# Kernel optimization log

Measured on AMD Instinct MI355X. Metric: run time of the kernel, lower is better.

Reference implementation:

```python
import jax, jax.numpy as jnp
import numpy as np

N_NODES = 100000
VOCAB = 5000
D = 256            # embedding_size
L = 4              # num_gnn_layers
E2 = 300000        # arity-2 hyperedges
E3 = 200000        # arity-3 hyperedges
T = 2000           # target nodes
N_LIN = 2          # num_linear_layer
EPS = 1e-5


def setup_inputs() -> dict:
    key = jax.random.key(0)
    ks = jax.random.split(key, 18)
    s = 0.02
    inp = {
        'x': jax.random.randint(ks[0], (N_NODES,), 0, VOCAB, dtype=jnp.int64) if jax.config.jax_enable_x64 else jax.random.randint(ks[0], (N_NODES,), 0, VOCAB).astype(jnp.int32),
        'edge_index': jax.random.randint(ks[1], (2, 500000), 0, N_NODES).astype(jnp.int32),
        'edge_list_arity2': jax.random.randint(ks[2], (2, E2), 0, N_NODES).astype(jnp.int32),
        'edge_list_arity3': jax.random.randint(ks[3], (3, E3), 0, N_NODES).astype(jnp.int32),
        'target_indices': jax.random.randint(ks[4], (T,), 0, N_NODES).astype(jnp.int32),
        # learned parameters
        'emb': jax.random.normal(ks[5], (VOCAB, D), jnp.float32),
        'W_root': jax.random.normal(ks[6], (L, D, D), jnp.float32) * s,
        'W_e2': jax.random.normal(ks[7], (L, 2 * D, 2 * D), jnp.float32) * s,
        'W_e3': jax.random.normal(ks[8], (L, 3 * D, 3 * D), jnp.float32) * s,
        'ln_g': jnp.ones((L, D), jnp.float32),
        'ln_b': jnp.zeros((L, D), jnp.float32),
        'reg_W': jax.random.normal(ks[9], (N_LIN, D, D), jnp.float32) * s,
        'reg_b': jnp.zeros((N_LIN, D), jnp.float32),
        'reg_ln_g': jnp.ones((N_LIN, D), jnp.float32),
        'reg_ln_b': jnp.zeros((N_LIN, D), jnp.float32),
        'out_W': jax.random.normal(ks[10], (D, 1), jnp.float32) * s,
        'out_b': jnp.zeros((1,), jnp.float32),
    }
    return inp


def _layernorm(h, g, b):
    mu = jnp.mean(h, axis=-1, keepdims=True)
    var = jnp.var(h, axis=-1, keepdims=True)
    return (h - mu) * jax.lax.rsqrt(var + EPS) * g + b


def _hyperconv(h, edge_idx, W_edge, W_root_l):
    # gather-transform-scatter for one edge type.
    # edge_idx: [arity, E]; h: [N, D]
    arity = edge_idx.shape[0]
    feats = h[edge_idx]                                  # [arity, E, D]
    cat = jnp.transpose(feats, (1, 0, 2)).reshape(-1, arity * h.shape[1])  # [E, arity*D]
    msg = cat @ W_edge                                   # [E, arity*D]
    msg = msg.reshape(-1, arity, h.shape[1])             # [E, arity, D]
    msg_flat = jnp.transpose(msg, (1, 0, 2)).reshape(-1, h.shape[1])       # [arity*E, D]
    agg = h @ W_root_l                                   # placeholder: caller adds; here return scatter only
    return edge_idx.reshape(-1), msg_flat


def reference(x, edge_index, edge_list_arity2, edge_list_arity3, target_indices,
              emb, W_root, W_e2, W_e3, ln_g, ln_b,
              reg_W, reg_b, reg_ln_g, reg_ln_b, out_W, out_b):
    h = emb[x]                                           # [N, D] embedding lookup
    for l in range(L):
        agg = h @ W_root[l]                              # self/root transform
        idx2, m2 = _hyperconv(h, edge_list_arity2, W_e2[l], W_root[l])
        agg = agg.at[idx2].add(m2)
        idx3, m3 = _hyperconv(h, edge_list_arity3, W_e3[l], W_root[l])
        agg = agg.at[idx3].add(m3)
        h = jax.nn.relu(agg)                             # conv internal activation
        h = _layernorm(h, ln_g[l], ln_b[l])              # inter_layer_norm
    out = h[target_indices]                              # [T, D]
    for i in range(N_LIN):
        out = _layernorm(out @ reg_W[i] + reg_b[i], reg_ln_g[i], reg_ln_b[i])
        out = jax.nn.relu(out)
    return out @ out_W + out_b                           # [T, 1] (label_size==2 -> 1 logit)
```

## Files before the change

kernel.cpp:

```cpp
#include <hip/hip_runtime.h>

typedef unsigned short u16;
typedef __bf16 bf16x8 __attribute__((ext_vector_type(8)));
typedef float f32x4 __attribute__((ext_vector_type(4)));

#define N_NODES 100000
#define D 256
#define NLAYER 4
#define E2N 300000
#define E3N 200000
#define TGT 2000

__device__ __forceinline__ u16 f2b(float f) {
    union { float f; unsigned u; } v; v.f = f;
    unsigned r = v.u + 0x7FFFu + ((v.u >> 16) & 1u);
    return (u16)(r >> 16);
}
__device__ __forceinline__ float b2f(u16 u) {
    union { unsigned u; float f; } v; v.u = ((unsigned)u) << 16; return v.f;
}

__device__ __forceinline__ void gload16(const void* g, void* l) {
    __builtin_amdgcn_global_load_lds(
        (const __attribute__((address_space(1))) void*)g,
        (__attribute__((address_space(3))) void*)l, 16, 0, 0);
}

__global__ __launch_bounds__(256)
void embed_kernel(const int* __restrict__ x, const float* __restrict__ emb,
                  u16* __restrict__ hb, int n) {
    int wid = threadIdx.x >> 6, lane = threadIdx.x & 63;
    int row = blockIdx.x * 4 + wid;
    if (row >= n) return;
    int v = x[row];
    float4 f = *(const float4*)(emb + v * D + lane * 4);
    ushort4 o; o.x = f2b(f.x); o.y = f2b(f.y); o.z = f2b(f.z); o.w = f2b(f.w);
    *(ushort4*)(hb + row * D + lane * 4) = o;
}

__global__ __launch_bounds__(256)
void convert_wt(const float* __restrict__ W, u16* __restrict__ Wt,
                int total, int K, int N) {
    int idx = blockIdx.x * 256 + threadIdx.x;
    if (idx >= total) return;
    int kk = idx % K;
    int rem = idx / K;
    int nn = rem % N;
    int l  = rem / N;
    Wt[idx] = f2b(W[(l * K + kk) * N + nn]);
}

__global__ __launch_bounds__(256)
void convert_cat(const float* __restrict__ W, u16* __restrict__ Wt,
                 int A, int total) {
    int idx = blockIdx.x * 256 + threadIdx.x;
    if (idx >= total) return;
    int k = idx & 255;
    int c = (idx >> 8) & 255;
    int r = idx >> 16;
    int t = r % A; int ls = r / A; int s = ls % A; int l = ls / A;
    int AD = A * 256;
    Wt[idx] = f2b(W[(size_t)(l * AD + t * 256 + k) * AD + s * 256 + c]);
}

#define NBINS 100000
#define NSEG 5
#define TOTENT 1200000
#define RPW (NBINS + 1)
#define NSTRIPE 16
#define SBINS (NBINS / NSTRIPE)
#define BPT 7

__global__ __launch_bounds__(256)
void zero_counts(int* __restrict__ counts) {
    int i = blockIdx.x * 256 + threadIdx.x;
    if (i < NSEG * NBINS) counts[i] = 0;
}

__device__ __forceinline__ void decode_entry(int i, const int* e2, const int* e3,
                                             int& seg, int& key, int& e, int& is2) {
    if (i < 2 * E2N) {
        int s = i / E2N; e = i - s * E2N;
        seg = s; key = e2[s * E2N + e]; is2 = 1;
    } else {
        int j = i - 2 * E2N; int s = j / E3N; e = j - s * E3N;
        seg = 2 + s; key = e3[s * E3N + e]; is2 = 0;
    }
}

__global__ __launch_bounds__(256)
void hist_kernel(const int* __restrict__ e2, const int* __restrict__ e3,
                 int* __restrict__ counts) {
    int i = blockIdx.x * 256 + threadIdx.x;
    if (i >= TOTENT) return;
    int seg, key, e, is2;
    decode_entry(i, e2, e3, seg, key, e, is2);
    atomicAdd(counts + seg * NBINS + key, 1);
}

__global__ __launch_bounds__(1024)
void scanA(int* __restrict__ counts, int* __restrict__ aux) {
    __shared__ int ps[1024];
    int* base = counts + (blockIdx.x / NSTRIPE) * NBINS + (blockIdx.x % NSTRIPE) * SBINS;
    int t = threadIdx.x;
    int b = t * BPT, en = b + BPT; if (en > SBINS) en = SBINS; if (b > SBINS) b = SBINS;
    int s = 0;
    for (int i = b; i < en; ++i) s += base[i];
    ps[t] = s; __syncthreads();
    for (int off = 1; off < 1024; off <<= 1) {
        int v = ps[t];
        if (t >= off) v += ps[t - off];
        __syncthreads();
        ps[t] = v; __syncthreads();
    }
    int run = (t == 0) ? 0 : ps[t - 1];
    for (int i = b; i < en; ++i) { int c = base[i]; base[i] = run; run += c; }
    if (t == 1023) aux[blockIdx.x] = ps[1023];
}

__global__ __launch_bounds__(256)
void scanB(int* __restrict__ aux) {
    int seg = threadIdx.x;
    if (seg >= NSEG) return;
    int run = 0;
    for (int i = 0; i < NSTRIPE; ++i) {
        int c = aux[seg * NSTRIPE + i];
        aux[seg * NSTRIPE + i] = run; run += c;
    }
}

__global__ __launch_bounds__(1024)
void scanC(int* __restrict__ counts, const int* __restrict__ aux) {
    int off = aux[blockIdx.x];
    if (off == 0) return;
    int* base = counts + (blockIdx.x / NSTRIPE) * NBINS + (blockIdx.x % NSTRIPE) * SBINS;
    int t = threadIdx.x;
    int b = t * BPT, en = b + BPT; if (en > SBINS) en = SBINS; if (b > SBINS) b = SBINS;
    for (int i = b; i < en; ++i) base[i] += off;
}

__global__ __launch_bounds__(256)
void copy_rowptr(const int* __restrict__ counts, int* __restrict__ rp) {
    int i = blockIdx.x * 256 + threadIdx.x;
    if (i >= NSEG * RPW) return;
    int seg = i / RPW, k = i - seg * RPW;
    rp[i] = (k < NBINS) ? counts[seg * NBINS + k] : (seg < 2 ? E2N : E3N);
}

__global__ __launch_bounds__(256)
void scatter_kernel(const int* __restrict__ e2, const int* __restrict__ e3,
                    int* __restrict__ counts, int* __restrict__ sorted2,
                    int* __restrict__ sorted3) {
    int i = blockIdx.x * 256 + threadIdx.x;
    if (i >= TOTENT) return;
    int seg, key, e, is2;
    decode_entry(i, e2, e3, seg, key, e, is2);
    int pos = atomicAdd(counts + seg * NBINS + key, 1);
    if (is2) sorted2[seg * E2N + pos] = e;
    else     sorted3[(seg - 2) * E3N + pos] = e;
}

__global__ __launch_bounds__(256)
void build_csrsrc(const int* __restrict__ src_ids, const int* __restrict__ csr,
                  int* __restrict__ out, int E) {
    int i = blockIdx.x * 256 + threadIdx.x;
    if (i >= E) return;
    out[i] = src_ids[csr[i]];
}

#define AP 264

template<int ARITY>
__global__ __launch_bounds__(512)
void fused_conv(const u16* __restrict__ hb, const int* __restrict__ csrsrc,
                const int* __restrict__ rp, const u16* __restrict__ Wl,
                float* __restrict__ agg, int E) {
    __shared__ __align__(16) u16 sA[64 * AP];
    const int m0 = blockIdx.x * 64;
    const int tid = threadIdx.x;
    const int lane = tid & 63;
    const int wid = tid >> 6;
    const int wcol = wid * 32;
    const int node0 = m0 + wid * 8;

    f32x4 acc[4][2];
#pragma unroll
    for (int i = 0; i < 4; ++i)
#pragma unroll
        for (int j = 0; j < 2; ++j)
            acc[i][j] = f32x4{0.f, 0.f, 0.f, 0.f};

#pragma unroll 1
    for (int s = 0; s < ARITY; ++s) {
        const int* rps = rp + s * RPW;
        int nidx = node0 + lane;
        nidx = (nidx > N_NODES) ? N_NODES : nidx;
        int rv = (lane <= 8) ? rps[nidx] : 0;
        const int ebase = __shfl(rv, 0);
        const int eend  = __shfl(rv, 8);
        const int nE    = eend - ebase;

#pragma unroll 1
        for (int t = 0; t < ARITY; ++t) {
            __syncthreads();
            if (t == s) {
#pragma unroll 1
                for (int r = 0; r < 8; ++r) {
                    int nl = wid * 8 + r;
                    int node = m0 + nl;
                    ushort4 o = {0, 0, 0, 0};
                    if (node < N_NODES) {
                        float dgf = (float)(__shfl(rv, r + 1) - __shfl(rv, r));
                        ushort4 h = *(const ushort4*)(hb + (size_t)node * 256 + lane * 4);
                        o.x = f2b(dgf * b2f(h.x)); o.y = f2b(dgf * b2f(h.y));
                        o.z = f2b(dgf * b2f(h.z)); o.w = f2b(dgf * b2f(h.w));
                    }
                    *(ushort4*)(sA + nl * AP + lane * 4) = o;
                }
            } else {
                const int* cs = csrsrc + (size_t)(s * ARITY + t) * E;
                int myi0 = (lane < nE) ? cs[ebase + lane] : 0;
                int myi1 = (lane + 64 < nE) ? cs[ebase + 64 + lane] : 0;

                int currow = 0;
                int rowend = __shfl(rv, 1) - ebase;
                float4 run = {0.f, 0.f, 0.f, 0.f};
#pragma unroll 1
                for (int eb = 0; eb < nE; eb += 8) {
                    ushort4 hv[8];
#pragma unroll
                    for (int j = 0; j < 8; ++j) {
                        int e = eb + j;
                        int src;
                        if (e >= nE)      src = 0;
                        else if (e < 64)  src = __shfl(myi0, e);
                        else if (e < 128) src = __shfl(myi1, e - 64);
                        else              src = cs[ebase + e];
                        hv[j] = *(const ushort4*)(hb + (size_t)src * 256 + lane * 4);
                    }
#pragma unroll
                    for (int j = 0; j < 8; ++j) {
                        int e = eb + j;
                        if (e < nE) {
                            while (e >= rowend) {
                                ushort4 o;
                                o.x = f2b(run.x); o.y = f2b(run.y);
                                o.z = f2b(run.z); o.w = f2b(run.w);
                                *(ushort4*)(sA + (wid * 8 + currow) * AP + lane * 4) = o;
                                run = float4{0.f, 0.f, 0.f, 0.f};
                                ++currow;
                                rowend = __shfl(rv, currow + 1) - ebase;
                            }
                            run.x += b2f(hv[j].x); run.y += b2f(hv[j].y);
                            run.z += b2f(hv[j].z); run.w += b2f(hv[j].w);
                        }
                    }
                }
                while (currow < 8) {
                    ushort4 o;
                    o.x = f2b(run.x); o.y = f2b(run.y);
                    o.z = f2b(run.z); o.w = f2b(run.w);
                    *(ushort4*)(sA + (wid * 8 + currow) * AP + lane * 4) = o;
                    run = float4{0.f, 0.f, 0.f, 0.f};
                    ++currow;
                }
            }
            __syncthreads();
            const u16* Bt = Wl + (size_t)(s * ARITY + t) * 65536;
#pragma unroll
            for (int k0 = 0; k0 < 256; k0 += 64) {
#pragma unroll
                for (int ks = 0; ks < 2; ++ks) {
                    const int koff = k0 + ks * 32 + (lane >> 4) * 8;
                    bf16x8 af[4], bf[2];
#pragma unroll
                    for (int mi = 0; mi < 4; ++mi)
                        af[mi] = *(const bf16x8*)(sA + (mi * 16 + (lane & 15)) * AP + koff);
#pragma unroll
                    for (int ni = 0; ni < 2; ++ni)
                        bf[ni] = *(const bf16x8*)(Bt + (size_t)(wcol + ni * 16 + (lane & 15)) * 256 + koff);
#pragma unroll
                    for (int mi = 0; mi < 4; ++mi)
#pragma unroll
                        for (int ni = 0; ni < 2; ++ni)
                            acc[mi][ni] = __builtin_amdgcn_mfma_f32_16x16x32_bf16(
                                af[mi], bf[ni], acc[mi][ni], 0, 0, 0);
                }
            }
        }
    }

    const int colb = wcol + (lane & 15);
#pragma unroll
    for (int mi = 0; mi < 4; ++mi) {
        int mbase = m0 + mi * 16 + ((lane >> 4) << 2);
#pragma unroll
        for (int r = 0; r < 4; ++r) {
            int m = mbase + r;
            if (m < N_NODES) {
#pragma unroll
                for (int ni = 0; ni < 2; ++ni)
                    agg[(size_t)m * 256 + colb + ni * 16] += acc[mi][ni][r];
            }
        }
    }
}

__global__ __launch_bounds__(256)
void gemm128(const u16* __restrict__ A, const u16* __restrict__ B,
             float* __restrict__ aggr, int M) {
    __shared__ __align__(16) u16 sA[128 * 64];
    __shared__ __align__(16) u16 sB[128 * 64];
    const int bid = blockIdx.x;
    const int mt = bid >> 1;
    const int nt = bid & 1;
    const int m0 = mt * 128;
    const int n0 = nt * 128;
    const int tid = threadIdx.x;
    const int lane = tid & 63;
    const int wid = tid >> 6;
    const int wm = (wid >> 1) * 64;
    const int wn = (wid & 1) * 64;
    const int lrow8 = lane >> 3;
    const int lcol  = (lane & 7) * 8;

    f32x4 acc[4][4];
#pragma unroll
    for (int i = 0; i < 4; ++i)
#pragma unroll
        for (int j = 0; j < 4; ++j)
            acc[i][j] = f32x4{0.f, 0.f, 0.f, 0.f};

    for (int k0 = 0; k0 < 256; k0 += 64) {
        __syncthreads();
#pragma unroll
        for (int i = 0; i < 4; ++i) {
            int row = wid * 32 + i * 8;
            int ar = m0 + row + lrow8; ar = (ar < M) ? ar : (M - 1);
            gload16(A + (size_t)ar * 256 + k0 + lcol, sA + row * 64);
            gload16(B + (size_t)(n0 + row + lrow8) * 256 + k0 + lcol, sB + row * 64);
        }
        __syncthreads();
#pragma unroll
        for (int ks = 0; ks < 2; ++ks) {
            const int koff = ks * 32 + (lane >> 4) * 8;
            bf16x8 af[4], bf[4];
#pragma unroll
            for (int mi = 0; mi < 4; ++mi)
                af[mi] = *(const bf16x8*)(sA + (wm + mi * 16 + (lane & 15)) * 64 + koff);
#pragma unroll
            for (int ni = 0; ni < 4; ++ni)
                bf[ni] = *(const bf16x8*)(sB + (wn + ni * 16 + (lane & 15)) * 64 + koff);
#pragma unroll
            for (int mi = 0; mi < 4; ++mi)
#pragma unroll
                for (int ni = 0; ni < 4; ++ni)
                    acc[mi][ni] = __builtin_amdgcn_mfma_f32_16x16x32_bf16(
                        af[mi], bf[ni], acc[mi][ni], 0, 0, 0);
        }
    }

    const int colb = n0 + wn + (lane & 15);
#pragma unroll
    for (int mi = 0; mi < 4; ++mi) {
        int mbase = m0 + wm + mi * 16 + ((lane >> 4) << 2);
#pragma unroll
        for (int r = 0; r < 4; ++r) {
            int m = mbase + r;
            if (m < M) {
#pragma unroll
                for (int ni = 0; ni < 4; ++ni)
                    aggr[(size_t)m * 256 + colb + ni * 16] = acc[mi][ni][r];
            }
        }
    }
}

__global__ __launch_bounds__(256)
void relu_ln_kernel(const float* __restrict__ agg, const float* __restrict__ g,
                    const float* __restrict__ b, u16* __restrict__ hb, int n) {
    int wid = threadIdx.x >> 6, lane = threadIdx.x & 63;
    int row = blockIdx.x * 4 + wid;
    if (row >= n) return;
    float4 v = *(const float4*)(agg + row * D + lane * 4);
    v.x = fmaxf(v.x, 0.f); v.y = fmaxf(v.y, 0.f);
    v.z = fmaxf(v.z, 0.f); v.w = fmaxf(v.w, 0.f);
    float s  = v.x + v.y + v.z + v.w;
    float s2 = v.x * v.x + v.y * v.y + v.z * v.z + v.w * v.w;
#pragma unroll
    for (int off = 1; off < 64; off <<= 1) {
        s  += __shfl_xor(s, off);
        s2 += __shfl_xor(s2, off);
    }
    float mu = s * 0.00390625f;
    float var = s2 * 0.00390625f - mu * mu;
    float rs = rsqrtf(var + 1e-5f);
    float4 gg = *(const float4*)(g + lane * 4);
    float4 bb = *(const float4*)(b + lane * 4);
    ushort4 o;
    o.x = f2b((v.x - mu) * rs * gg.x + bb.x);
    o.y = f2b((v.y - mu) * rs * gg.y + bb.y);
    o.z = f2b((v.z - mu) * rs * gg.z + bb.z);
    o.w = f2b((v.w - mu) * rs * gg.w + bb.w);
    *(ushort4*)(hb + row * D + lane * 4) = o;
}

__global__ __launch_bounds__(256)
void head_layer(const u16* __restrict__ hb, const int* __restrict__ tgt,
                const float* __restrict__ inf,
                const float* __restrict__ W, const float* __restrict__ bias,
                const float* __restrict__ g, const float* __restrict__ beta,
                float* __restrict__ out, int gather) {
    __shared__ float xr[256];
    __shared__ float sm1[4], sm2[4];
    int t = blockIdx.x, tid = threadIdx.x;
    if (gather) { int node = tgt[t]; xr[tid] = b2f(hb[node * D + tid]); }
    else        { xr[tid] = inf[t * D + tid]; }
    __syncthreads();
    float a = bias[tid];
#pragma unroll 8
    for (int k = 0; k < 256; ++k) a = fmaf(xr[k], W[k * 256 + tid], a);
    float s = a, s2 = a * a;
#pragma unroll
    for (int off = 1; off < 64; off <<= 1) {
        s  += __shfl_xor(s, off);
        s2 += __shfl_xor(s2, off);
    }
    int wid = tid >> 6, lane = tid & 63;
    if (lane == 0) { sm1[wid] = s; sm2[wid] = s2; }
    __syncthreads();
    s  = sm1[0] + sm1[1] + sm1[2] + sm1[3];
    s2 = sm2[0] + sm2[1] + sm2[2] + sm2[3];
    float mu = s * 0.00390625f;
    float var = s2 * 0.00390625f - mu * mu;
    float rs = rsqrtf(var + 1e-5f);
    float y = (a - mu) * rs * g[tid] + beta[tid];
    out[t * 256 + tid] = fmaxf(y, 0.f);
}

__global__ __launch_bounds__(256)
void head_out(const float* __restrict__ in, const float* __restrict__ ow,
              const float* __restrict__ ob, float* __restrict__ out, int T) {
    int wid = threadIdx.x >> 6, lane = threadIdx.x & 63;
    int t = blockIdx.x * 4 + wid;
    if (t >= T) return;
    float4 v = *(const float4*)(in + t * D + lane * 4);
    float4 w = *(const float4*)(ow + lane * 4);
    float s = v.x * w.x + v.y * w.y + v.z * w.z + v.w * w.w;
#pragma unroll
    for (int off = 1; off < 64; off <<= 1) s += __shfl_xor(s, off);
    if (lane == 0) out[t] = s + ob[0];
}

extern "C" void kernel_launch(void* const* d_in, const int* in_sizes, int n_in,
                              void* d_out, int out_size, void* d_ws, size_t ws_size,
                              hipStream_t stream) {
    (void)in_sizes; (void)n_in; (void)out_size; (void)ws_size;
    const int*   x      = (const int*)d_in[0];
    const int*   e2     = (const int*)d_in[2];
    const int*   e3     = (const int*)d_in[3];
    const int*   tgt    = (const int*)d_in[4];
    const float* emb    = (const float*)d_in[5];
    const float* W_root = (const float*)d_in[6];
    const float* W_e2   = (const float*)d_in[7];
    const float* W_e3   = (const float*)d_in[8];
    const float* ln_g   = (const float*)d_in[9];
    const float* ln_b   = (const float*)d_in[10];
    const float* reg_W  = (const float*)d_in[11];
    const float* reg_b  = (const float*)d_in[12];
    const float* rln_g  = (const float*)d_in[13];
    const float* rln_b  = (const float*)d_in[14];
    const float* out_W  = (const float*)d_in[15];
    const float* out_b  = (const float*)d_in[16];
    float* out = (float*)d_out;

    char* ws = (char*)d_ws;
    float* agg     = (float*)(ws);
    int*   counts  = (int*)  (ws);
    u16*   hb      = (u16*)  (ws + 102400000);
    u16*   Wr      = (u16*)  (ws + 153600000);
    u16*   W2c     = (u16*)  (ws + 154124288);
    u16*   W3c     = (u16*)  (ws + 156221440);
    int*   sorted2 = (int*)  (ws + 160940032);
    int*   sorted3 = (int*)  (ws + 163340032);
    int*   rp      = (int*)  (ws + 165740032);
    int*   aux     = (int*)  (ws + 167740160);
    int*   csrsrc2 = (int*)  (ws + 167741184);
    int*   csrsrc3 = (int*)  (ws + 172541184);
    float* t0      = (float*)(ws + 179741184);
    float* t1      = (float*)(ws + 181789184);

    embed_kernel<<<N_NODES / 4, 256, 0, stream>>>(x, emb, hb, N_NODES);
    convert_wt<<<(NLAYER * 256 * 256 + 255) / 256, 256, 0, stream>>>(W_root, Wr, NLAYER * 256 * 256, 256, 256);
    convert_cat<<<(NLAYER * 4 * 65536 + 255) / 256, 256, 0, stream>>>(W_e2, W2c, 2, NLAYER * 4 * 65536);
    convert_cat<<<(NLAYER * 9 * 65536 + 255) / 256, 256, 0, stream>>>(W_e3, W3c, 3, NLAYER * 9 * 65536);

    zero_counts<<<(NSEG * NBINS + 255) / 256, 256, 0, stream>>>(counts);
    hist_kernel<<<(TOTENT + 255) / 256, 256, 0, stream>>>(e2, e3, counts);
    scanA<<<NSEG * NSTRIPE, 1024, 0, stream>>>(counts, aux);
    scanB<<<1, 256, 0, stream>>>(aux);
    scanC<<<NSEG * NSTRIPE, 1024, 0, stream>>>(counts, aux);
    copy_rowptr<<<(NSEG * RPW + 255) / 256, 256, 0, stream>>>(counts, rp);
    scatter_kernel<<<(TOTENT + 255) / 256, 256, 0, stream>>>(e2, e3, counts, sorted2, sorted3);

    for (int s = 0; s < 2; ++s)
        for (int t = 0; t < 2; ++t)
            build_csrsrc<<<(E2N + 255) / 256, 256, 0, stream>>>(
                e2 + (size_t)t * E2N, sorted2 + (size_t)s * E2N,
                csrsrc2 + (size_t)(s * 2 + t) * E2N, E2N);
    for (int s = 0; s < 3; ++s)
        for (int t = 0; t < 3; ++t)
            build_csrsrc<<<(E3N + 255) / 256, 256, 0, stream>>>(
                e3 + (size_t)t * E3N, sorted3 + (size_t)s * E3N,
                csrsrc3 + (size_t)(s * 3 + t) * E3N, E3N);

    const int mgrid = ((N_NODES + 127) / 128) * 2;
    const int fgrid = (N_NODES + 63) / 64;

    for (int l = 0; l < NLAYER; ++l) {
        gemm128<<<mgrid, 256, 0, stream>>>(hb, Wr + (size_t)l * 65536, agg, N_NODES);
        fused_conv<2><<<fgrid, 512, 0, stream>>>(
            hb, csrsrc2, rp, W2c + (size_t)l * 4 * 65536, agg, E2N);
        fused_conv<3><<<fgrid, 512, 0, stream>>>(
            hb, csrsrc3, rp + 2 * RPW, W3c + (size_t)l * 9 * 65536, agg, E3N);
        relu_ln_kernel<<<N_NODES / 4, 256, 0, stream>>>(agg, ln_g + l * D, ln_b + l * D, hb, N_NODES);
    }

    head_layer<<<TGT, 256, 0, stream>>>(hb, tgt, nullptr, reg_W, reg_b, rln_g, rln_b, t0, 1);
    head_layer<<<TGT, 256, 0, stream>>>(nullptr, nullptr, t0, reg_W + 65536, reg_b + 256, rln_g + 256, rln_b + 256, t1, 0);
    head_out<<<(TGT + 3) / 4, 256, 0, stream>>>(t1, out_W, out_b, out, TGT);
}
```

Measured before the change: 3.365 ms.

## Fuse root GEMM, both hyperconvs, ReLU and LayerNorm into one per-layer kernel

Replaces the per-layer sequence of root GEMM, two fused_conv kernels and a relu+layernorm kernel with a single fused_layer kernel. It runs 14 phases (root, four arity-2 and nine arity-3 blocks) that accumulate into one register tile, then applies ReLU and a cross-wave LayerNorm reduction in shared memory and writes bf16 h directly. This removes the fp32 agg buffer round trips (write, read-modify-write twice, read) and several launches. It ping-pongs h between two buffers. The trade-offs are that the root GEMM now uses the less efficient per-block path, the fused kernel may use more registers, and occupancy is bounded to 6.

```diff
diff --git a/kernel.cpp b/kernel.cpp
--- a/kernel.cpp
+++ b/kernel.cpp
@@ -18,12 +18,6 @@
 }
 __device__ __forceinline__ float b2f(u16 u) {
     union { unsigned u; float f; } v; v.u = ((unsigned)u) << 16; return v.f;
-}
-
-__device__ __forceinline__ void gload16(const void* g, void* l) {
-    __builtin_amdgcn_global_load_lds(
-        (const __attribute__((address_space(1))) void*)g,
-        (__attribute__((address_space(3))) void*)l, 16, 0, 0);
 }
 
 __global__ __launch_bounds__(256)
@@ -170,12 +164,16 @@
 
 #define AP 264
 
-template<int ARITY>
-__global__ __launch_bounds__(512)
-void fused_conv(const u16* __restrict__ hb, const int* __restrict__ csrsrc,
-                const int* __restrict__ rp, const u16* __restrict__ Wl,
-                float* __restrict__ agg, int E) {
+__global__ __launch_bounds__(512, 6)
+void fused_layer(const u16* __restrict__ hin, u16* __restrict__ hout,
+                 const int* __restrict__ csrsrc2, const int* __restrict__ csrsrc3,
+                 const int* __restrict__ rp,
+                 const u16* __restrict__ Wr_l, const u16* __restrict__ W2_l,
+                 const u16* __restrict__ W3_l,
+                 const float* __restrict__ lng, const float* __restrict__ lnb) {
     __shared__ __align__(16) u16 sA[64 * AP];
+    __shared__ float lnS[64][8];
+    __shared__ float lnS2[64][8];
     const int m0 = blockIdx.x * 64;
     const int tid = threadIdx.x;
     const int lane = tid & 63;
@@ -191,218 +189,183 @@
             acc[i][j] = f32x4{0.f, 0.f, 0.f, 0.f};
 
 #pragma unroll 1
-    for (int s = 0; s < ARITY; ++s) {
-        const int* rps = rp + s * RPW;
-        int nidx = node0 + lane;
-        nidx = (nidx > N_NODES) ? N_NODES : nidx;
-        int rv = (lane <= 8) ? rps[nidx] : 0;
-        const int ebase = __shfl(rv, 0);
-        const int eend  = __shfl(rv, 8);
-        const int nE    = eend - ebase;
-
+    for (int ph = 0; ph < 14; ++ph) {
+        int type, s, t;
+        if (ph == 0)      { type = 0; s = 0; t = 0; }
+        else if (ph <= 4) { int p = ph - 1; type = 2; s = p >> 1; t = p & 1; }
+        else              { int p = ph - 5; type = 3; s = p / 3; t = p - (p / 3) * 3; }
+
+        const int* rps = nullptr;
+        const int* cs  = nullptr;
+        const u16* Bt;
+        int E = 0;
+        if (type == 0) {
+            Bt = Wr_l;
+        } else if (type == 2) {
+            rps = rp + s * RPW; E = E2N;
+            cs = csrsrc2 + (size_t)(s * 2 + t) * E2N;
+            Bt = W2_l + (size_t)(s * 2 + t) * 65536;
+        } else {
+            rps = rp + (2 + s) * RPW; E = E3N;
+            cs = csrsrc3 + (size_t)(s * 3 + t) * E3N;
+            Bt = W3_l + (size_t)(s * 3 + t) * 65536;
+        }
+
+        int rv = 0, ebase = 0, nE = 0;
+        if (type != 0) {
+            int nidx = node0 + lane;
+            nidx = (nidx > N_NODES) ? N_NODES : nidx;
+            rv = (lane <= 8) ? rps[nidx] : 0;
+            ebase = __shfl(rv, 0);
+            nE = __shfl(rv, 8) - ebase;
+        }
+
+        __syncthreads();
+        if (type == 0 || t == s) {
 #pragma unroll 1
-        for (int t = 0; t < ARITY; ++t) {
-            __syncthreads();
-            if (t == s) {
+            for (int r = 0; r < 8; ++r) {
+                int nl = wid * 8 + r;
+                int node = m0 + nl;
+                ushort4 o = {0, 0, 0, 0};
+                if (node < N_NODES) {
+                    float dgf = (type == 0) ? 1.f
+                              : (float)(__shfl(rv, r + 1) - __shfl(rv, r));
+                    ushort4 h = *(const ushort4*)(hin + (size_t)node * 256 + lane * 4);
+                    o.x = f2b(dgf * b2f(h.x)); o.y = f2b(dgf * b2f(h.y));
+                    o.z = f2b(dgf * b2f(h.z)); o.w = f2b(dgf * b2f(h.w));
+                }
+                *(ushort4*)(sA + nl * AP + lane * 4) = o;
+            }
+        } else {
+            int myi0 = (lane < nE) ? cs[ebase + lane] : 0;
+            int myi1 = (lane + 64 < nE) ? cs[ebase + 64 + lane] : 0;
+
+            int currow = 0;
+            int rowend = __shfl(rv, 1) - ebase;
+            float4 run = {0.f, 0.f, 0.f, 0.f};
 #pragma unroll 1
-                for (int r = 0; r < 8; ++r) {
-                    int nl = wid * 8 + r;
-                    int node = m0 + nl;
-                    ushort4 o = {0, 0, 0, 0};
-                    if (node < N_NODES) {
-                        float dgf = (float)(__shfl(rv, r + 1) - __shfl(rv, r));
-                        ushort4 h = *(const ushort4*)(hb + (size_t)node * 256 + lane * 4);
-                        o.x = f2b(dgf * b2f(h.x)); o.y = f2b(dgf * b2f(h.y));
-                        o.z = f2b(dgf * b2f(h.z)); o.w = f2b(dgf * b2f(h.w));
-                    }
-                    *(ushort4*)(sA + nl * AP + lane * 4) = o;
+            for (int eb = 0; eb < nE; eb += 8) {
+                ushort4 hv[8];
+#pragma unroll
+                for (int j = 0; j < 8; ++j) {
+                    int e = eb + j;
+                    int src;
+                    if (e >= nE)      src = 0;
+                    else if (e < 64)  src = __shfl(myi0, e);
+                    else if (e < 128) src = __shfl(myi1, e - 64);
+                    else              src = cs[ebase + e];
+                    hv[j] = *(const ushort4*)(hin + (size_t)src * 256 + lane * 4);
                 }
-            } else {
-                const int* cs = csrsrc + (size_t)(s * ARITY + t) * E;
-                int myi0 = (lane < nE) ? cs[ebase + lane] : 0;
-                int myi1 = (lane + 64 < nE) ? cs[ebase + 64 + lane] : 0;
-
-                int currow = 0;
-                int rowend = __shfl(rv, 1) - ebase;
-                float4 run = {0.f, 0.f, 0.f, 0.f};
-#pragma unroll 1
-                for (int eb = 0; eb < nE; eb += 8) {
-                    ushort4 hv[8];
-#pragma unroll
-                    for (int j = 0; j < 8; ++j) {
-                        int e = eb + j;
-                        int src;
-                        if (e >= nE)      src = 0;
-                        else if (e < 64)  src = __shfl(myi0, e);
-                        else if (e < 128) src = __shfl(myi1, e - 64);
-                        else              src = cs[ebase + e];
-                        hv[j] = *(const ushort4*)(hb + (size_t)src * 256 + lane * 4);
-                    }
-#pragma unroll
-                    for (int j = 0; j < 8; ++j) {
-                        int e = eb + j;
-                        if (e < nE) {
-                            while (e >= rowend) {
-                                ushort4 o;
-                                o.x = f2b(run.x); o.y = f2b(run.y);
-                                o.z = f2b(run.z); o.w = f2b(run.w);
-                                *(ushort4*)(sA + (wid * 8 + currow) * AP + lane * 4) = o;
-                                run = float4{0.f, 0.f, 0.f, 0.f};
-                                ++currow;
-                                rowend = __shfl(rv, currow + 1) - ebase;
-                            }
-                            run.x += b2f(hv[j].x); run.y += b2f(hv[j].y);
-                            run.z += b2f(hv[j].z); run.w += b2f(hv[j].w);
+#pragma unroll
+                for (int j = 0; j < 8; ++j) {
+                    int e = eb + j;
+                    if (e < nE) {
+                        while (e >= rowend) {
+                            ushort4 o;
+                            o.x = f2b(run.x); o.y = f2b(run.y);
+                            o.z = f2b(run.z); o.w = f2b(run.w);
+                            *(ushort4*)(sA + (wid * 8 + currow) * AP + lane * 4) = o;
+                            run = float4{0.f, 0.f, 0.f, 0.f};
+                            ++currow;
+                            rowend = __shfl(rv, currow + 1) - ebase;
                         }
+                        run.x += b2f(hv[j].x); run.y += b2f(hv[j].y);
+                        run.z += b2f(hv[j].z); run.w += b2f(hv[j].w);
                     }
                 }
-                while (currow < 8) {
-                    ushort4 o;
-                    o.x = f2b(run.x); o.y = f2b(run.y);
-                    o.z = f2b(run.z); o.w = f2b(run.w);
-                    *(ushort4*)(sA + (wid * 8 + currow) * AP + lane * 4) = o;
-                    run = float4{0.f, 0.f, 0.f, 0.f};
-                    ++currow;
-                }
-            }
-            __syncthreads();
-            const u16* Bt = Wl + (size_t)(s * ARITY + t) * 65536;
-#pragma unroll
-            for (int k0 = 0; k0 < 256; k0 += 64) {
-#pragma unroll
-                for (int ks = 0; ks < 2; ++ks) {
-                    const int koff = k0 + ks * 32 + (lane >> 4) * 8;
-                    bf16x8 af[4], bf[2];
-#pragma unroll
-                    for (int mi = 0; mi < 4; ++mi)
-                        af[mi] = *(const bf16x8*)(sA + (mi * 16 + (lane & 15)) * AP + koff);
+            }
+            while (currow < 8) {
+                ushort4 o;
+                o.x = f2b(run.x); o.y = f2b(run.y);
+                o.z = f2b(run.z); o.w = f2b(run.w);
+                *(ushort4*)(sA + (wid * 8 + currow) * AP + lane * 4) = o;
+                run = float4{0.f, 0.f, 0.f, 0.f};
+                ++currow;
+            }
+        }
+        __syncthreads();
+#pragma unroll
+        for (int k0 = 0; k0 < 256; k0 += 64) {
+#pragma unroll
+            for (int ks = 0; ks < 2; ++ks) {
+                const int koff = k0 + ks * 32 + (lane >> 4) * 8;
+                bf16x8 af[4], bf[2];
+#pragma unroll
+                for (int mi = 0; mi < 4; ++mi)
+                    af[mi] = *(const bf16x8*)(sA + (mi * 16 + (lane & 15)) * AP + koff);
+#pragma unroll
+                for (int ni = 0; ni < 2; ++ni)
+                    bf[ni] = *(const bf16x8*)(Bt + (size_t)(wcol + ni * 16 + (lane & 15)) * 256 + koff);
+#pragma unroll
+                for (int mi = 0; mi < 4; ++mi)
 #pragma unroll
                     for (int ni = 0; ni < 2; ++ni)
-                        bf[ni] = *(const bf16x8*)(Bt + (size_t)(wcol + ni * 16 + (lane & 15)) * 256 + koff);
-#pragma unroll
-                    for (int mi = 0; mi < 4; ++mi)
-#pragma unroll
-                        for (int ni = 0; ni < 2; ++ni)
-                            acc[mi][ni] = __builtin_amdgcn_mfma_f32_16x16x32_bf16(
-                                af[mi], bf[ni], acc[mi][ni], 0, 0, 0);
-                }
-            }
-        }
-    }
-
-    const int colb = wcol + (lane & 15);
+                        acc[mi][ni] = __builtin_amdgcn_mfma_f32_16x16x32_bf16(
+                            af[mi], bf[ni], acc[mi][ni], 0, 0, 0);
+            }
+        }
+    }
+
+#pragma unroll
+    for (int mi = 0; mi < 4; ++mi)
+#pragma unroll
+        for (int ni = 0; ni < 2; ++ni)
+#pragma unroll
+            for (int r = 0; r < 4; ++r)
+                acc[mi][ni][r] = fmaxf(acc[mi][ni][r], 0.f);
+
+    const int q = lane >> 4;
 #pragma unroll
     for (int mi = 0; mi < 4; ++mi) {
-        int mbase = m0 + mi * 16 + ((lane >> 4) << 2);
 #pragma unroll
         for (int r = 0; r < 4; ++r) {
-            int m = mbase + r;
-            if (m < N_NODES) {
-#pragma unroll
-                for (int ni = 0; ni < 2; ++ni)
-                    agg[(size_t)m * 256 + colb + ni * 16] += acc[mi][ni][r];
-            }
-        }
-    }
-}
-
-__global__ __launch_bounds__(256)
-void gemm128(const u16* __restrict__ A, const u16* __restrict__ B,
-             float* __restrict__ aggr, int M) {
-    __shared__ __align__(16) u16 sA[128 * 64];
-    __shared__ __align__(16) u16 sB[128 * 64];
-    const int bid = blockIdx.x;
-    const int mt = bid >> 1;
-    const int nt = bid & 1;
-    const int m0 = mt * 128;
-    const int n0 = nt * 128;
-    const int tid = threadIdx.x;
-    const int lane = tid & 63;
-    const int wid = tid >> 6;
-    const int wm = (wid >> 1) * 64;
-    const int wn = (wid & 1) * 64;
-    const int lrow8 = lane >> 3;
-    const int lcol  = (lane & 7) * 8;
-
-    f32x4 acc[4][4];
-#pragma unroll
-    for (int i = 0; i < 4; ++i)
-#pragma unroll
-        for (int j = 0; j < 4; ++j)
-            acc[i][j] = f32x4{0.f, 0.f, 0.f, 0.f};
-
-    for (int k0 = 0; k0 < 256; k0 += 64) {
-        __syncthreads();
-#pragma unroll
-        for (int i = 0; i < 4; ++i) {
-            int row = wid * 32 + i * 8;
-            int ar = m0 + row + lrow8; ar = (ar < M) ? ar : (M - 1);
-            gload16(A + (size_t)ar * 256 + k0 + lcol, sA + row * 64);
-            gload16(B + (size_t)(n0 + row + lrow8) * 256 + k0 + lcol, sB + row * 64);
-        }
-        __syncthreads();
-#pragma unroll
-        for (int ks = 0; ks < 2; ++ks) {
-            const int koff = ks * 32 + (lane >> 4) * 8;
-            bf16x8 af[4], bf[4];
-#pragma unroll
-            for (int mi = 0; mi < 4; ++mi)
-                af[mi] = *(const bf16x8*)(sA + (wm + mi * 16 + (lane & 15)) * 64 + koff);
-#pragma unroll
-            for (int ni = 0; ni < 4; ++ni)
-                bf[ni] = *(const bf16x8*)(sB + (wn + ni * 16 + (lane & 15)) * 64 + koff);
-#pragma unroll
-            for (int mi = 0; mi < 4; ++mi)
-#pragma unroll
-                for (int ni = 0; ni < 4; ++ni)
-                    acc[mi][ni] = __builtin_amdgcn_mfma_f32_16x16x32_bf16(
-                        af[mi], bf[ni], acc[mi][ni], 0, 0, 0);
-        }
-    }
-
-    const int colb = n0 + wn + (lane & 15);
+            float p1 = acc[mi][0][r] + acc[mi][1][r];
+            float p2 = acc[mi][0][r] * acc[mi][0][r] + acc[mi][1][r] * acc[mi][1][r];
+#pragma unroll
+            for (int off = 1; off < 16; off <<= 1) {
+                p1 += __shfl_xor(p1, off);
+                p2 += __shfl_xor(p2, off);
+            }
+            if ((lane & 15) == 0) {
+                int rl = mi * 16 + q * 4 + r;
+                lnS[rl][wid] = p1; lnS2[rl][wid] = p2;
+            }
+        }
+    }
+    __syncthreads();
+    const float g0 = lng[wcol + (lane & 15)];
+    const float g1 = lng[wcol + 16 + (lane & 15)];
+    const float b0 = lnb[wcol + (lane & 15)];
+    const float b1 = lnb[wcol + 16 + (lane & 15)];
 #pragma unroll
     for (int mi = 0; mi < 4; ++mi) {
-        int mbase = m0 + wm + mi * 16 + ((lane >> 4) << 2);
 #pragma unroll
         for (int r = 0; r < 4; ++r) {
-            int m = mbase + r;
-            if (m < M) {
-#pragma unroll
-                for (int ni = 0; ni < 4; ++ni)
-                    aggr[(size_t)m * 256 + colb + ni * 16] = acc[mi][ni][r];
-            }
-        }
-    }
-}
-
-__global__ __launch_bounds__(256)
-void relu_ln_kernel(const float* __restrict__ agg, const float* __restrict__ g,
-                    const float* __restrict__ b, u16* __restrict__ hb, int n) {
-    int wid = threadIdx.x >> 6, lane = threadIdx.x & 63;
-    int row = blockIdx.x * 4 + wid;
-    if (row >= n) return;
-    float4 v = *(const float4*)(agg + row * D + lane * 4);
-    v.x = fmaxf(v.x, 0.f); v.y = fmaxf(v.y, 0.f);
-    v.z = fmaxf(v.z, 0.f); v.w = fmaxf(v.w, 0.f);
-    float s  = v.x + v.y + v.z + v.w;
-    float s2 = v.x * v.x + v.y * v.y + v.z * v.z + v.w * v.w;
-#pragma unroll
-    for (int off = 1; off < 64; off <<= 1) {
-        s  += __shfl_xor(s, off);
-        s2 += __shfl_xor(s2, off);
-    }
-    float mu = s * 0.00390625f;
-    float var = s2 * 0.00390625f - mu * mu;
-    float rs = rsqrtf(var + 1e-5f);
-    float4 gg = *(const float4*)(g + lane * 4);
-    float4 bb = *(const float4*)(b + lane * 4);
-    ushort4 o;
-    o.x = f2b((v.x - mu) * rs * gg.x + bb.x);
-    o.y = f2b((v.y - mu) * rs * gg.y + bb.y);
-    o.z = f2b((v.z - mu) * rs * gg.z + bb.z);
-    o.w = f2b((v.w - mu) * rs * gg.w + bb.w);
-    *(ushort4*)(hb + row * D + lane * 4) = o;
+            int rl = mi * 16 + q * 4 + r;
+            float s1 = 0.f, s2 = 0.f;
+#pragma unroll
+            for (int w = 0; w < 8; ++w) { s1 += lnS[rl][w]; s2 += lnS2[rl][w]; }
+            float mu = s1 * 0.00390625f;
+            float var = s2 * 0.00390625f - mu * mu;
+            float rs = rsqrtf(var + 1e-5f);
+            float y0 = (acc[mi][0][r] - mu) * rs * g0 + b0;
+            float y1 = (acc[mi][1][r] - mu) * rs * g1 + b1;
+            sA[rl * AP + wcol + (lane & 15)]      = f2b(y0);
+            sA[rl * AP + wcol + 16 + (lane & 15)] = f2b(y1);
+        }
+    }
+    __syncthreads();
+    {
+        int row = tid >> 3;
+        int node = m0 + row;
+        if (node < N_NODES) {
+            int c0 = (tid & 7) * 32;
+#pragma unroll
+            for (int j = 0; j < 4; ++j)
+                *(uint4*)(hout + (size_t)node * 256 + c0 + j * 8) =
+                    *(const uint4*)(sA + row * AP + c0 + j * 8);
+        }
+    }
 }
 
 __global__ __launch_bounds__(256)
@@ -475,9 +438,9 @@
     float* out = (float*)d_out;
 
     char* ws = (char*)d_ws;
-    float* agg     = (float*)(ws);
     int*   counts  = (int*)  (ws);
-    u16*   hb      = (u16*)  (ws + 102400000);
+    u16*   hb1     = (u16*)  (ws);
+    u16*   hb0     = (u16*)  (ws + 102400000);
     u16*   Wr      = (u16*)  (ws + 153600000);
     u16*   W2c     = (u16*)  (ws + 154124288);
     u16*   W3c     = (u16*)  (ws + 156221440);
@@ -490,7 +453,7 @@
     float* t0      = (float*)(ws + 179741184);
     float* t1      = (float*)(ws + 181789184);
 
-    embed_kernel<<<N_NODES / 4, 256, 0, stream>>>(x, emb, hb, N_NODES);
+    embed_kernel<<<N_NODES / 4, 256, 0, stream>>>(x, emb, hb0, N_NODES);
     convert_wt<<<(NLAYER * 256 * 256 + 255) / 256, 256, 0, stream>>>(W_root, Wr, NLAYER * 256 * 256, 256, 256);
     convert_cat<<<(NLAYER * 4 * 65536 + 255) / 256, 256, 0, stream>>>(W_e2, W2c, 2, NLAYER * 4 * 65536);
     convert_cat<<<(NLAYER * 9 * 65536 + 255) / 256, 256, 0, stream>>>(W_e3, W3c, 3, NLAYER * 9 * 65536);
@@ -514,19 +477,20 @@
                 e3 + (size_t)t * E3N, sorted3 + (size_t)s * E3N,
                 csrsrc3 + (size_t)(s * 3 + t) * E3N, E3N);
 
-    const int mgrid = ((N_NODES + 127) / 128) * 2;
     const int fgrid = (N_NODES + 63) / 64;
-
+    u16* hbuf[2] = { hb0, hb1 };
     for (int l = 0; l < NLAYER; ++l) {
-        gemm128<<<mgrid, 256, 0, stream>>>(hb, Wr + (size_t)l * 65536, agg, N_NODES);
-        fused_conv<2><<<fgrid, 512, 0, stream>>>(
-            hb, csrsrc2, rp, W2c + (size_t)l * 4 * 65536, agg, E2N);
-        fused_conv<3><<<fgrid, 512, 0, stream>>>(
-            hb, csrsrc3, rp + 2 * RPW, W3c + (size_t)l * 9 * 65536, agg, E3N);
-        relu_ln_kernel<<<N_NODES / 4, 256, 0, stream>>>(agg, ln_g + l * D, ln_b + l * D, hb, N_NODES);
-    }
-
-    head_layer<<<TGT, 256, 0, stream>>>(hb, tgt, nullptr, reg_W, reg_b, rln_g, rln_b, t0, 1);
+        u16* hin  = hbuf[l & 1];
+        u16* hout = hbuf[(l & 1) ^ 1];
+        fused_layer<<<fgrid, 512, 0, stream>>>(
+            hin, hout, csrsrc2, csrsrc3, rp,
+            Wr  + (size_t)l * 65536,
+            W2c + (size_t)l * 4 * 65536,
+            W3c + (size_t)l * 9 * 65536,
+            ln_g + l * D, ln_b + l * D);
+    }
+
+    head_layer<<<TGT, 256, 0, stream>>>(hb0, tgt, nullptr, reg_W, reg_b, rln_g, rln_b, t0, 1);
     head_layer<<<TGT, 256, 0, stream>>>(nullptr, nullptr, t0, reg_W + 65536, reg_b + 256, rln_g + 256, rln_b + 256, t1, 0);
     head_out<<<(TGT + 3) / 4, 256, 0, stream>>>(t1, out_W, out_b, out, TGT);
 }
```

Result: faster. 2.900 ms (-13.8%).
